# Kernel tuning notes

Hardware: AMD Instinct MI355X
Metric: run time of the kernel (lower is better)

The kernel has to match this reference:

```python
import jax, jax.numpy as jnp
import numpy as np

DIM = 1024
HEADS = 16
WIN = 128
MLP_HIDDEN = int(DIM * 2.0)
EPS = 1e-5


def setup_inputs() -> dict:
    key = jax.random.key(0)
    ks = jax.random.split(key, 8)
    s = lambda k, shape, scale=0.02: jax.random.normal(k, shape, dtype=jnp.float32) * scale
    return {
        'x': jax.random.normal(ks[0], (4, 8192, DIM), dtype=jnp.float32),
        'ln1_w': jnp.ones((DIM,), jnp.float32), 'ln1_b': jnp.zeros((DIM,), jnp.float32),
        'qkv_w': s(ks[1], (3 * DIM, DIM)), 'qkv_b': jnp.zeros((3 * DIM,), jnp.float32),
        'proj_w': s(ks[2], (DIM, DIM)), 'proj_b': jnp.zeros((DIM,), jnp.float32),
        'ln2_w': jnp.ones((DIM,), jnp.float32), 'ln2_b': jnp.zeros((DIM,), jnp.float32),
        'fc1_w': s(ks[3], (MLP_HIDDEN, DIM)), 'fc1_b': jnp.zeros((MLP_HIDDEN,), jnp.float32),
        'fc2_w': s(ks[4], (DIM, MLP_HIDDEN)), 'fc2_b': jnp.zeros((DIM,), jnp.float32),
    }


def _layernorm(x, w, b):
    mu = jnp.mean(x, axis=-1, keepdims=True)
    var = jnp.mean(jnp.square(x - mu), axis=-1, keepdims=True)
    return (x - mu) * jax.lax.rsqrt(var + EPS) * w + b


def _windowed_attn(x, qkv_w, qkv_b, proj_w, proj_b):
    B, N, C = x.shape
    H, D = HEADS, C // HEADS
    qkv = x @ qkv_w.T + qkv_b                       # (B,N,3C)
    qkv = qkv.reshape(B, N, 3, H, D).transpose(2, 0, 3, 1, 4)  # (3,B,H,N,D)
    q, k, v = qkv[0], qkv[1], qkv[2]
    pad = (WIN - N % WIN) % WIN
    if pad:
        padw = ((0, 0), (0, 0), (0, pad), (0, 0))
        q = jnp.pad(q, padw); k = jnp.pad(k, padw); v = jnp.pad(v, padw)
    Np = q.shape[2]
    W = Np // WIN
    q = q.reshape(B, H, W, WIN, D)
    k = k.reshape(B, H, W, WIN, D)
    v = v.reshape(B, H, W, WIN, D)
    attn = jnp.einsum('bhwqd,bhwkd->bhwqk', q, k) * (D ** -0.5)
    attn = jax.nn.softmax(attn, axis=-1)
    out = jnp.einsum('bhwqk,bhwkd->bhwqd', attn, v)
    out = out.reshape(B, H, Np, D)[:, :, :N, :]
    out = out.transpose(0, 2, 1, 3).reshape(B, N, C)
    return out @ proj_w.T + proj_b


def reference(x, ln1_w, ln1_b, qkv_w, qkv_b, proj_w, proj_b, ln2_w, ln2_b, fc1_w, fc1_b, fc2_w, fc2_b):
    x = x + _windowed_attn(_layernorm(x, ln1_w, ln1_b), qkv_w, qkv_b, proj_w, proj_b)
    h = _layernorm(x, ln2_w, ln2_b)
    h = jax.nn.gelu(h @ fc1_w.T + fc1_b, approximate=False)
    return x + (h @ fc2_w.T + fc2_b)
```

## Files before the change

### kernel.cpp

```cpp
#include <hip/hip_runtime.h>
#include <hip/hip_bf16.h>
#include <math.h>

#define AS1 __attribute__((address_space(1)))
#define AS3 __attribute__((address_space(3)))

typedef __bf16 bf16;
typedef __bf16 bf16x2 __attribute__((ext_vector_type(2)));
typedef __bf16 bf16x4 __attribute__((ext_vector_type(4)));
typedef __bf16 bf16x8 __attribute__((ext_vector_type(8)));
typedef float  f32x4  __attribute__((ext_vector_type(4)));

#define DIM   1024
#define MLPH  2048
#define HEADS 16
#define HD    64
#define WIN   128
#define NBAT  4
#define SEQ   8192
#define MTOK  (NBAT*SEQ)

__device__ __forceinline__ void gload_lds16(const void* g, void* l) {
  __builtin_amdgcn_global_load_lds((const AS1 void*)g, (AS3 void*)l, 16, 0, 0);
}

__global__ __launch_bounds__(256) void cvt_w(const float* __restrict__ in,
                                             bf16* __restrict__ out, int n4) {
  int i = blockIdx.x * 256 + threadIdx.x;
  if (i < n4) {
    float4 v = ((const float4*)in)[i];
    bf16x4 o;
    o[0] = (bf16)v.x; o[1] = (bf16)v.y; o[2] = (bf16)v.z; o[3] = (bf16)v.w;
    ((bf16x4*)out)[i] = o;
  }
}

__global__ __launch_bounds__(256) void ln_bf16(const float* __restrict__ x,
                                               const float* __restrict__ w,
                                               const float* __restrict__ b,
                                               bf16* __restrict__ out) {
  int row = blockIdx.x;
  int t = threadIdx.x;
  float4 v = ((const float4*)(x + (size_t)row * DIM))[t];
  float s  = v.x + v.y + v.z + v.w;
  float ss = v.x*v.x + v.y*v.y + v.z*v.z + v.w*v.w;
#pragma unroll
  for (int off = 32; off; off >>= 1) { s += __shfl_xor(s, off); ss += __shfl_xor(ss, off); }
  __shared__ float sb[8];
  int wid = t >> 6, lane = t & 63;
  if (!lane) { sb[wid] = s; sb[wid + 4] = ss; }
  __syncthreads();
  s  = sb[0] + sb[1] + sb[2] + sb[3];
  ss = sb[4] + sb[5] + sb[6] + sb[7];
  float mu = s * (1.0f / DIM);
  float rs = rsqrtf(ss * (1.0f / DIM) - mu * mu + 1e-5f);
  float4 wv = ((const float4*)w)[t];
  float4 bv = ((const float4*)b)[t];
  bf16x4 o;
  o[0] = (bf16)((v.x - mu) * rs * wv.x + bv.x);
  o[1] = (bf16)((v.y - mu) * rs * wv.y + bv.y);
  o[2] = (bf16)((v.z - mu) * rs * wv.z + bv.z);
  o[3] = (bf16)((v.w - mu) * rs * wv.w + bv.w);
  ((bf16x4*)(out + (size_t)row * DIM))[t] = o;
}

template<int N, int K, int EPI>
__global__ __launch_bounds__(256) void gemm_bt(const bf16* __restrict__ A,
                                               const bf16* __restrict__ Bw,
                                               const float* __restrict__ bias,
                                               const float* __restrict__ resid,
                                               void* __restrict__ Cout) {
  __shared__ alignas(16) bf16 As[128 * 64];
  __shared__ alignas(16) bf16 Bs[128 * 64];
  const int tid = threadIdx.x;
  const int wid = tid >> 6;
  const int lane = tid & 63;
  const int wm = wid >> 1, wn = wid & 1;
  const int m0 = blockIdx.y * 128;
  const int n0 = blockIdx.x * 128;

  f32x4 acc[4][4] = {};

  const char* Ab = (const char*)A;
  const char* Bb = (const char*)Bw;
  const int o_base = (wid << 12) + lane * 16;

  for (int k0 = 0; k0 < K; k0 += 64) {
#pragma unroll
    for (int r = 0; r < 4; ++r) {
      int o = o_base + (r << 10);
      int row = o >> 7;
      int cb = (o & 127) ^ ((row & 7) << 4);
      gload_lds16(Ab + ((size_t)(m0 + row) * K + k0) * 2 + cb,
                  (char*)As + (wid << 12) + (r << 10));
      gload_lds16(Bb + ((size_t)(n0 + row) * K + k0) * 2 + cb,
                  (char*)Bs + (wid << 12) + (r << 10));
    }
    __syncthreads();
#pragma unroll
    for (int kk = 0; kk < 2; ++kk) {
      bf16x8 af[4], bfr[4];
      int cb = (kk << 6) + ((lane >> 4) << 4);
#pragma unroll
      for (int i = 0; i < 4; ++i) {
        int rA = (wm << 6) + (i << 4) + (lane & 15);
        af[i] = *(const bf16x8*)((const char*)As + rA * 128 + (cb ^ ((rA & 7) << 4)));
        int rB = (wn << 6) + (i << 4) + (lane & 15);
        bfr[i] = *(const bf16x8*)((const char*)Bs + rB * 128 + (cb ^ ((rB & 7) << 4)));
      }
#pragma unroll
      for (int i = 0; i < 4; ++i)
#pragma unroll
        for (int j = 0; j < 4; ++j)
          acc[i][j] = __builtin_amdgcn_mfma_f32_16x16x32_bf16(af[i], bfr[j], acc[i][j], 0, 0, 0);
    }
    __syncthreads();
  }

  const int lr = (lane >> 4) << 2;
  const int lc = lane & 15;
#pragma unroll
  for (int i = 0; i < 4; ++i) {
#pragma unroll
    for (int j = 0; j < 4; ++j) {
      int row = m0 + (wm << 6) + (i << 4) + lr;
      int col = n0 + (wn << 6) + (j << 4) + lc;
      float bv = bias[col];
#pragma unroll
      for (int r = 0; r < 4; ++r) {
        size_t idx = (size_t)(row + r) * N + col;
        float v = acc[i][j][r] + bv;
        if constexpr (EPI == 0) {
          ((bf16*)Cout)[idx] = (bf16)v;
        } else if constexpr (EPI == 1) {
          ((float*)Cout)[idx] = v + resid[idx];
        } else {
          float g = 0.5f * v * (1.0f + erff(v * 0.70710678118654752f));
          ((bf16*)Cout)[idx] = (bf16)g;
        }
      }
    }
  }
}

__global__ __launch_bounds__(256) void attn_win(const bf16* __restrict__ qkv,
                                                bf16* __restrict__ out) {
  __shared__ alignas(16) char smem[49152];
  bf16* Qs = (bf16*)smem;
  bf16* Ks = (bf16*)(smem + 16384);
  bf16* Vt = (bf16*)(smem + 32768);

  const int tid = threadIdx.x, wid = tid >> 6, lane = tid & 63;
  const int bid = blockIdx.x;
  const int w = bid & 63, h = (bid >> 6) & 15, b = bid >> 10;
  const size_t tok0 = (size_t)b * SEQ + (size_t)w * WIN;
  const char* qbase = (const char*)(qkv + tok0 * 3072 + h * 64);

#pragma unroll
  for (int r = 0; r < 4; ++r) {
    int o = (wid << 12) + (r << 10) + lane * 16;
    int row = o >> 7;
    int cb = (o & 127) ^ ((row & 7) << 4);
    const char* g = qbase + (size_t)row * 6144 + cb;
    gload_lds16(g,        smem + (wid << 12) + (r << 10));
    gload_lds16(g + 2048, smem + 16384 + (wid << 12) + (r << 10));
  }
  {
    int k0 = (tid & 63) * 2;
    int dblk = (tid >> 6) * 16;
    const bf16* s0 = qkv + (tok0 + k0) * 3072 + 2048 + h * 64 + dblk;
    bf16x8 r0a = *(const bf16x8*)s0;
    bf16x8 r0b = *(const bf16x8*)(s0 + 8);
    bf16x8 r1a = *(const bf16x8*)(s0 + 3072);
    bf16x8 r1b = *(const bf16x8*)(s0 + 3072 + 8);
#pragma unroll
    for (int e = 0; e < 8; ++e) {
      int d = dblk + e;
      bf16x2 p; p[0] = r0a[e]; p[1] = r1a[e];
      *(bf16x2*)((char*)Vt + d * 256 + ((2 * k0) ^ ((d & 7) << 4))) = p;
      int d2 = dblk + 8 + e;
      bf16x2 p2; p2[0] = r0b[e]; p2[1] = r1b[e];
      *(bf16x2*)((char*)Vt + d2 * 256 + ((2 * k0) ^ ((d2 & 7) << 4))) = p2;
    }
  }
  __syncthreads();

  f32x4 s[2][8] = {};
#pragma unroll
  for (int kk = 0; kk < 2; ++kk) {
    bf16x8 aq[2], bk[8];
    int cb = (kk << 6) + ((lane >> 4) << 4);
#pragma unroll
    for (int i = 0; i < 2; ++i) {
      int rA = (wid << 5) + (i << 4) + (lane & 15);
      aq[i] = *(const bf16x8*)((const char*)Qs + rA * 128 + (cb ^ ((rA & 7) << 4)));
    }
#pragma unroll
    for (int j = 0; j < 8; ++j) {
      int rB = (j << 4) + (lane & 15);
      bk[j] = *(const bf16x8*)((const char*)Ks + rB * 128 + (cb ^ ((rB & 7) << 4)));
    }
#pragma unroll
    for (int i = 0; i < 2; ++i)
#pragma unroll
      for (int j = 0; j < 8; ++j)
        s[i][j] = __builtin_amdgcn_mfma_f32_16x16x32_bf16(aq[i], bk[j], s[i][j], 0, 0, 0);
  }
  __syncthreads();

  float rcp[2][4];
#pragma unroll
  for (int i = 0; i < 2; ++i) {
#pragma unroll
    for (int r = 0; r < 4; ++r) {
      float mx = -1e30f;
#pragma unroll
      for (int j = 0; j < 8; ++j) { s[i][j][r] *= 0.125f; mx = fmaxf(mx, s[i][j][r]); }
#pragma unroll
      for (int off = 8; off; off >>= 1) mx = fmaxf(mx, __shfl_xor(mx, off));
      float sum = 0.f;
#pragma unroll
      for (int j = 0; j < 8; ++j) { float p = __expf(s[i][j][r] - mx); s[i][j][r] = p; sum += p; }
#pragma unroll
      for (int off = 8; off; off >>= 1) sum += __shfl_xor(sum, off);
      rcp[i][r] = 1.f / sum;
    }
  }

  bf16* Pw = (bf16*)(smem + (wid << 13));
#pragma unroll
  for (int i = 0; i < 2; ++i)
#pragma unroll
    for (int j = 0; j < 8; ++j)
#pragma unroll
      for (int r = 0; r < 4; ++r) {
        int pr = (i << 4) + ((lane >> 4) << 2) + r;
        int pc = (j << 4) + (lane & 15);
        *(bf16*)((char*)Pw + pr * 256 + ((2 * pc) ^ ((pr & 7) << 4))) = (bf16)s[i][j][r];
      }

  f32x4 oacc[2][4] = {};
#pragma unroll
  for (int kk = 0; kk < 4; ++kk) {
    bf16x8 ap[2], bv[4];
    int cb = (kk << 6) + ((lane >> 4) << 4);
#pragma unroll
    for (int i = 0; i < 2; ++i) {
      int pr = (i << 4) + (lane & 15);
      ap[i] = *(const bf16x8*)((const char*)Pw + pr * 256 + (cb ^ ((pr & 7) << 4)));
    }
#pragma unroll
    for (int n = 0; n < 4; ++n) {
      int vr = (n << 4) + (lane & 15);
      bv[n] = *(const bf16x8*)((const char*)Vt + vr * 256 + (cb ^ ((vr & 7) << 4)));
    }
#pragma unroll
    for (int i = 0; i < 2; ++i)
#pragma unroll
      for (int n = 0; n < 4; ++n)
        oacc[i][n] = __builtin_amdgcn_mfma_f32_16x16x32_bf16(ap[i], bv[n], oacc[i][n], 0, 0, 0);
  }

#pragma unroll
  for (int i = 0; i < 2; ++i)
#pragma unroll
    for (int n = 0; n < 4; ++n)
#pragma unroll
      for (int r = 0; r < 4; ++r) {
        int q = (wid << 5) + (i << 4) + ((lane >> 4) << 2) + r;
        int d = (n << 4) + (lane & 15);
        out[(tok0 + q) * 1024 + h * 64 + d] = (bf16)(oacc[i][n][r] * rcp[i][r]);
      }
}

extern "C" void kernel_launch(void* const* d_in, const int* in_sizes, int n_in,
                              void* d_out, int out_size, void* d_ws, size_t ws_size,
                              hipStream_t stream) {
  const float* x     = (const float*)d_in[0];
  const float* ln1w  = (const float*)d_in[1];
  const float* ln1b  = (const float*)d_in[2];
  const float* qkvw  = (const float*)d_in[3];
  const float* qkvb  = (const float*)d_in[4];
  const float* projw = (const float*)d_in[5];
  const float* projb = (const float*)d_in[6];
  const float* ln2w  = (const float*)d_in[7];
  const float* ln2b  = (const float*)d_in[8];
  const float* fc1w  = (const float*)d_in[9];
  const float* fc1b  = (const float*)d_in[10];
  const float* fc2w  = (const float*)d_in[11];
  const float* fc2b  = (const float*)d_in[12];
  float* out = (float*)d_out;

  char* ws = (char*)d_ws;
  bf16* lnbuf = (bf16*)ws;
  bf16* qkv   = (bf16*)(ws + ((size_t)64 << 20));
  bf16* attnb = lnbuf;
  bf16* hbuf  = qkv;
  bf16* wq    = (bf16*)(ws + ((size_t)256 << 20));
  bf16* wp    = wq + 3072 * 1024;
  bf16* w1    = wp + 1024 * 1024;
  bf16* w2    = w1 + 2048 * 1024;

  cvt_w<<<3072, 256, 0, stream>>>(qkvw, wq, 3072 * 1024 / 4);
  cvt_w<<<1024, 256, 0, stream>>>(projw, wp, 1024 * 1024 / 4);
  cvt_w<<<2048, 256, 0, stream>>>(fc1w, w1, 2048 * 1024 / 4);
  cvt_w<<<2048, 256, 0, stream>>>(fc2w, w2, 1024 * 2048 / 4);

  ln_bf16<<<MTOK, 256, 0, stream>>>(x, ln1w, ln1b, lnbuf);
  gemm_bt<3072, 1024, 0><<<dim3(24, 256), 256, 0, stream>>>(lnbuf, wq, qkvb, nullptr, qkv);
  attn_win<<<4096, 256, 0, stream>>>(qkv, attnb);
  gemm_bt<1024, 1024, 1><<<dim3(8, 256), 256, 0, stream>>>(attnb, wp, projb, x, out);
  ln_bf16<<<MTOK, 256, 0, stream>>>(out, ln2w, ln2b, lnbuf);
  gemm_bt<2048, 1024, 2><<<dim3(16, 256), 256, 0, stream>>>(lnbuf, w1, fc1b, nullptr, hbuf);
  gemm_bt<1024, 2048, 1><<<dim3(8, 256), 256, 0, stream>>>(hbuf, w2, fc2b, out, out);
}
```

Baseline: 1.182 ms.

## Replace 128x128 GEMM with double-buffered 256x256 tile, 8-wave pipelined kernel

```diff
diff --git a/kernel.cpp b/kernel.cpp
--- a/kernel.cpp
+++ b/kernel.cpp
@@ -12,9 +12,7 @@
 typedef float  f32x4  __attribute__((ext_vector_type(4)));
 
 #define DIM   1024
-#define MLPH  2048
 #define HEADS 16
-#define HD    64
 #define WIN   128
 #define NBAT  4
 #define SEQ   8192
@@ -64,72 +62,132 @@
   ((bf16x4*)(out + (size_t)row * DIM))[t] = o;
 }
 
+#define MFMA16(base_)                                                          \
+  _Pragma("unroll") for (int kk = 0; kk < 2; ++kk)                             \
+  _Pragma("unroll") for (int i = 0; i < 2; ++i)                                \
+  _Pragma("unroll") for (int nj = 0; nj < 4; ++nj)                             \
+    acc[(base_) + i][nj] = __builtin_amdgcn_mfma_f32_16x16x32_bf16(            \
+        afrag[i][kk], bfrag[nj][kk], acc[(base_) + i][nj], 0, 0, 0);
+
+#define READ_A(i_, mi_) {                                                      \
+    int rA_ = wm * 128 + (mi_) * 16 + fr;                                      \
+    afrag[i_][0] = *(const bf16x8*)(Ab_ + rA_ * 128 + ((fcb)      ^ fsw));     \
+    afrag[i_][1] = *(const bf16x8*)(Ab_ + rA_ * 128 + ((64 + fcb) ^ fsw)); }
+
 template<int N, int K, int EPI>
-__global__ __launch_bounds__(256) void gemm_bt(const bf16* __restrict__ A,
-                                               const bf16* __restrict__ Bw,
-                                               const float* __restrict__ bias,
-                                               const float* __restrict__ resid,
-                                               void* __restrict__ Cout) {
-  __shared__ alignas(16) bf16 As[128 * 64];
-  __shared__ alignas(16) bf16 Bs[128 * 64];
+__global__ __launch_bounds__(512, 2) void gemm256(const bf16* __restrict__ A,
+                                                  const bf16* __restrict__ Bw,
+                                                  const float* __restrict__ bias,
+                                                  const float* __restrict__ resid,
+                                                  void* __restrict__ Cout) {
+  extern __shared__ char lds[];
+  constexpr int NT = K / 64;
+  constexpr int K2 = K * 2;
   const int tid = threadIdx.x;
-  const int wid = tid >> 6;
-  const int lane = tid & 63;
-  const int wm = wid >> 1, wn = wid & 1;
-  const int m0 = blockIdx.y * 128;
-  const int n0 = blockIdx.x * 128;
-
-  f32x4 acc[4][4] = {};
-
-  const char* Ab = (const char*)A;
-  const char* Bb = (const char*)Bw;
-  const int o_base = (wid << 12) + lane * 16;
-
-  for (int k0 = 0; k0 < K; k0 += 64) {
-#pragma unroll
-    for (int r = 0; r < 4; ++r) {
-      int o = o_base + (r << 10);
-      int row = o >> 7;
-      int cb = (o & 127) ^ ((row & 7) << 4);
-      gload_lds16(Ab + ((size_t)(m0 + row) * K + k0) * 2 + cb,
-                  (char*)As + (wid << 12) + (r << 10));
-      gload_lds16(Bb + ((size_t)(n0 + row) * K + k0) * 2 + cb,
-                  (char*)Bs + (wid << 12) + (r << 10));
-    }
-    __syncthreads();
-#pragma unroll
-    for (int kk = 0; kk < 2; ++kk) {
-      bf16x8 af[4], bfr[4];
-      int cb = (kk << 6) + ((lane >> 4) << 4);
-#pragma unroll
-      for (int i = 0; i < 4; ++i) {
-        int rA = (wm << 6) + (i << 4) + (lane & 15);
-        af[i] = *(const bf16x8*)((const char*)As + rA * 128 + (cb ^ ((rA & 7) << 4)));
-        int rB = (wn << 6) + (i << 4) + (lane & 15);
-        bfr[i] = *(const bf16x8*)((const char*)Bs + rB * 128 + (cb ^ ((rB & 7) << 4)));
-      }
-#pragma unroll
-      for (int i = 0; i < 4; ++i)
-#pragma unroll
-        for (int j = 0; j < 4; ++j)
-          acc[i][j] = __builtin_amdgcn_mfma_f32_16x16x32_bf16(af[i], bfr[j], acc[i][j], 0, 0, 0);
-    }
-    __syncthreads();
-  }
-
-  const int lr = (lane >> 4) << 2;
-  const int lc = lane & 15;
-#pragma unroll
-  for (int i = 0; i < 4; ++i) {
-#pragma unroll
-    for (int j = 0; j < 4; ++j) {
-      int row = m0 + (wm << 6) + (i << 4) + lr;
-      int col = n0 + (wn << 6) + (j << 4) + lc;
+  const int w = tid >> 6, lane = tid & 63;
+  const int wm = w >> 2, wn = w & 3;
+  const int m0 = blockIdx.y * 256, n0 = blockIdx.x * 256;
+
+  const int srow = lane >> 3;
+  const int ssw  = ((lane & 7) ^ srow) << 4;
+  const char* Asrc = (const char*)A + (size_t)(m0 + srow) * K2 + ssw;
+  const char* Bsrc = (const char*)Bw + (size_t)(n0 + srow) * K2 + ssw;
+
+  const int fr  = lane & 15;
+  const int fcb = (lane >> 4) << 4;
+  const int fsw = (fr & 7) << 4;
+
+  f32x4 acc[8][4] = {};
+
+  {
+    char* A0 = lds;
+    char* B0 = lds + 32768;
+    char* B1 = lds + 65536 + 32768;
+    gload_lds16(Asrc + (size_t)((w     ) * 8) * K2, A0 + (w     ) * 1024);
+    gload_lds16(Asrc + (size_t)((16 + w) * 8) * K2, A0 + (16 + w) * 1024);
+    gload_lds16(Asrc + (size_t)((8  + w) * 8) * K2, A0 + (8  + w) * 1024);
+    gload_lds16(Asrc + (size_t)((24 + w) * 8) * K2, A0 + (24 + w) * 1024);
+    gload_lds16(Bsrc + (size_t)((w     ) * 8) * K2, B0 + (w     ) * 1024);
+    gload_lds16(Bsrc + (size_t)((8  + w) * 8) * K2, B0 + (8  + w) * 1024);
+    gload_lds16(Bsrc + (size_t)((16 + w) * 8) * K2, B0 + (16 + w) * 1024);
+    gload_lds16(Bsrc + (size_t)((24 + w) * 8) * K2, B0 + (24 + w) * 1024);
+    const size_t k1 = (NT > 1 ? 1 : 0) * 128;
+    gload_lds16(Bsrc + (size_t)((w     ) * 8) * K2 + k1, B1 + (w     ) * 1024);
+    gload_lds16(Bsrc + (size_t)((8  + w) * 8) * K2 + k1, B1 + (8  + w) * 1024);
+    gload_lds16(Bsrc + (size_t)((16 + w) * 8) * K2 + k1, B1 + (16 + w) * 1024);
+    gload_lds16(Bsrc + (size_t)((24 + w) * 8) * K2 + k1, B1 + (24 + w) * 1024);
+    asm volatile("s_waitcnt vmcnt(4)" ::: "memory");
+    __builtin_amdgcn_s_barrier();
+  }
+
+#pragma unroll 1
+  for (int t = 0; t < NT; ++t) {
+    const char* Ab_ = lds + (t & 1) * 65536;
+    const char* Bb_ = Ab_ + 32768;
+    char* An = lds + ((t + 1) & 1) * 65536;
+    char* Bn = lds + (t & 1) * 65536 + 32768;
+    const size_t ka = (size_t)((t + 1 < NT) ? t + 1 : NT - 1) * 128;
+    const size_t kb = (size_t)((t + 2 < NT) ? t + 2 : NT - 1) * 128;
+
+    bf16x8 bfrag[4][2], afrag[2][2];
+
+#pragma unroll
+    for (int nj = 0; nj < 4; ++nj) {
+      int rB = wn * 64 + nj * 16 + fr;
+      bfrag[nj][0] = *(const bf16x8*)(Bb_ + rB * 128 + ((fcb)      ^ fsw));
+      bfrag[nj][1] = *(const bf16x8*)(Bb_ + rB * 128 + ((64 + fcb) ^ fsw));
+    }
+    READ_A(0, 0) READ_A(1, 1)
+    gload_lds16(Asrc + (size_t)((w     ) * 8) * K2 + ka, An + (w     ) * 1024);
+    gload_lds16(Asrc + (size_t)((16 + w) * 8) * K2 + ka, An + (16 + w) * 1024);
+    __builtin_amdgcn_s_barrier();
+    __builtin_amdgcn_s_setprio(1);
+    MFMA16(0)
+    __builtin_amdgcn_s_setprio(0);
+    __builtin_amdgcn_s_barrier();
+
+    READ_A(0, 2) READ_A(1, 3)
+    gload_lds16(Asrc + (size_t)((8  + w) * 8) * K2 + ka, An + (8  + w) * 1024);
+    gload_lds16(Asrc + (size_t)((24 + w) * 8) * K2 + ka, An + (24 + w) * 1024);
+    __builtin_amdgcn_s_barrier();
+    __builtin_amdgcn_s_setprio(1);
+    MFMA16(2)
+    __builtin_amdgcn_s_setprio(0);
+    asm volatile("s_waitcnt vmcnt(8)" ::: "memory");
+    __builtin_amdgcn_s_barrier();
+
+    READ_A(0, 4) READ_A(1, 5)
+    gload_lds16(Bsrc + (size_t)((w     ) * 8) * K2 + kb, Bn + (w     ) * 1024);
+    gload_lds16(Bsrc + (size_t)((8  + w) * 8) * K2 + kb, Bn + (8  + w) * 1024);
+    __builtin_amdgcn_s_barrier();
+    __builtin_amdgcn_s_setprio(1);
+    MFMA16(4)
+    __builtin_amdgcn_s_setprio(0);
+    __builtin_amdgcn_s_barrier();
+
+    READ_A(0, 6) READ_A(1, 7)
+    gload_lds16(Bsrc + (size_t)((16 + w) * 8) * K2 + kb, Bn + (16 + w) * 1024);
+    gload_lds16(Bsrc + (size_t)((24 + w) * 8) * K2 + kb, Bn + (24 + w) * 1024);
+    __builtin_amdgcn_s_barrier();
+    __builtin_amdgcn_s_setprio(1);
+    MFMA16(6)
+    __builtin_amdgcn_s_setprio(0);
+    asm volatile("s_waitcnt vmcnt(6)" ::: "memory");
+    __builtin_amdgcn_s_barrier();
+  }
+
+  const int lr4 = (lane >> 4) << 2;
+#pragma unroll
+  for (int mi = 0; mi < 8; ++mi) {
+#pragma unroll
+    for (int nj = 0; nj < 4; ++nj) {
+      int row = m0 + wm * 128 + mi * 16 + lr4;
+      int col = n0 + wn * 64 + nj * 16 + fr;
       float bv = bias[col];
 #pragma unroll
       for (int r = 0; r < 4; ++r) {
         size_t idx = (size_t)(row + r) * N + col;
-        float v = acc[i][j][r] + bv;
+        float v = acc[mi][nj][r] + bv;
         if constexpr (EPI == 0) {
           ((bf16*)Cout)[idx] = (bf16)v;
         } else if constexpr (EPI == 1) {
@@ -146,8 +204,6 @@
 __global__ __launch_bounds__(256) void attn_win(const bf16* __restrict__ qkv,
                                                 bf16* __restrict__ out) {
   __shared__ alignas(16) char smem[49152];
-  bf16* Qs = (bf16*)smem;
-  bf16* Ks = (bf16*)(smem + 16384);
   bf16* Vt = (bf16*)(smem + 32768);
 
   const int tid = threadIdx.x, wid = tid >> 6, lane = tid & 63;
@@ -193,12 +249,12 @@
 #pragma unroll
     for (int i = 0; i < 2; ++i) {
       int rA = (wid << 5) + (i << 4) + (lane & 15);
-      aq[i] = *(const bf16x8*)((const char*)Qs + rA * 128 + (cb ^ ((rA & 7) << 4)));
+      aq[i] = *(const bf16x8*)(smem + rA * 128 + (cb ^ ((rA & 7) << 4)));
     }
 #pragma unroll
     for (int j = 0; j < 8; ++j) {
       int rB = (j << 4) + (lane & 15);
-      bk[j] = *(const bf16x8*)((const char*)Ks + rB * 128 + (cb ^ ((rB & 7) << 4)));
+      bk[j] = *(const bf16x8*)(smem + 16384 + rB * 128 + (cb ^ ((rB & 7) << 4)));
     }
 #pragma unroll
     for (int i = 0; i < 2; ++i)
@@ -301,16 +357,21 @@
   bf16* w1    = wp + 1024 * 1024;
   bf16* w2    = w1 + 2048 * 1024;
 
+  hipFuncSetAttribute((const void*)gemm256<3072, 1024, 0>, hipFuncAttributeMaxDynamicSharedMemorySize, 131072);
+  hipFuncSetAttribute((const void*)gemm256<1024, 1024, 1>, hipFuncAttributeMaxDynamicSharedMemorySize, 131072);
+  hipFuncSetAttribute((const void*)gemm256<2048, 1024, 2>, hipFuncAttributeMaxDynamicSharedMemorySize, 131072);
+  hipFuncSetAttribute((const void*)gemm256<1024, 2048, 1>, hipFuncAttributeMaxDynamicSharedMemorySize, 131072);
+
   cvt_w<<<3072, 256, 0, stream>>>(qkvw, wq, 3072 * 1024 / 4);
   cvt_w<<<1024, 256, 0, stream>>>(projw, wp, 1024 * 1024 / 4);
   cvt_w<<<2048, 256, 0, stream>>>(fc1w, w1, 2048 * 1024 / 4);
   cvt_w<<<2048, 256, 0, stream>>>(fc2w, w2, 1024 * 2048 / 4);
 
   ln_bf16<<<MTOK, 256, 0, stream>>>(x, ln1w, ln1b, lnbuf);
-  gemm_bt<3072, 1024, 0><<<dim3(24, 256), 256, 0, stream>>>(lnbuf, wq, qkvb, nullptr, qkv);
+  gemm256<3072, 1024, 0><<<dim3(12, 128), 512, 131072, stream>>>(lnbuf, wq, qkvb, nullptr, qkv);
   attn_win<<<4096, 256, 0, stream>>>(qkv, attnb);
-  gemm_bt<1024, 1024, 1><<<dim3(8, 256), 256, 0, stream>>>(attnb, wp, projb, x, out);
+  gemm256<1024, 1024, 1><<<dim3(4, 128), 512, 131072, stream>>>(attnb, wp, projb, x, out);
   ln_bf16<<<MTOK, 256, 0, stream>>>(out, ln2w, ln2b, lnbuf);
-  gemm_bt<2048, 1024, 2><<<dim3(16, 256), 256, 0, stream>>>(lnbuf, w1, fc1b, nullptr, hbuf);
-  gemm_bt<1024, 2048, 1><<<dim3(8, 256), 256, 0, stream>>>(hbuf, w2, fc2b, out, out);
-}
+  gemm256<2048, 1024, 2><<<dim3(8, 128), 512, 131072, stream>>>(lnbuf, w1, fc1b, nullptr, hbuf);
+  gemm256<1024, 2048, 1><<<dim3(4, 128), 512, 131072, stream>>>(hbuf, w2, fc2b, out, out);
+}
```

Measured after the change: 1.019 ms. 1.16x faster.
